# Kernel tuning notes

Measured on AMD Instinct MI355X. Metric: run time of the kernel, lower is better.

Reference implementation:

```python
import jax, jax.numpy as jnp
import numpy as np

N_NODES = 100000
N_EDGES = 3200000
DIM = 64


def setup_inputs() -> dict:
    key = jax.random.key(0)
    k1, k2, k3, k4 = jax.random.split(key, 4)
    features = jax.random.normal(k1, (N_NODES, DIM), dtype=jnp.float32)
    attn_w = jax.random.normal(k2, (2 * DIM,), dtype=jnp.float32) / np.sqrt(2 * DIM)
    src = jax.random.randint(k3, (N_EDGES,), 0, N_NODES, dtype=jnp.int32)
    dst = jax.random.randint(k4, (N_EDGES,), 0, N_NODES, dtype=jnp.int32)
    return {"features": features, "attn_w": attn_w, "src": src, "dst": dst}


def reference(features, attn_w, src, dst):
    n = features.shape[0]
    d = features.shape[1]
    a_src, a_dst = attn_w[:d], attn_w[d:]
    # Edge attention: leaky_relu(Linear(concat(h_src, h_dst))) == leaky_relu(h_src@a_src + h_dst@a_dst)
    s_src = features @ a_src  # [N]
    s_dst = features @ a_dst  # [N]
    e = jax.nn.leaky_relu(s_src[src] + s_dst[dst], negative_slope=0.01)  # [E]
    # Segment softmax over incoming edges of each destination node
    emax = jax.ops.segment_max(e, dst, num_segments=n)  # [N], -inf for isolated nodes
    ee = jnp.exp(e - emax[dst])  # [E]
    denom = jax.ops.segment_sum(ee, dst, num_segments=n)  # [N]
    alpha = ee / denom[dst]  # [E]
    # Weighted neighbor aggregation (gather src feats, scatter-add into dst)
    h = jax.ops.segment_sum(alpha[:, None] * features[src], dst, num_segments=n)  # [N, D]
    return jax.nn.elu(h)
```

## Files before the change

kernel.cpp:

```cpp
#include <hip/hip_runtime.h>
#include <math.h>

#define DIM 64
#define SCAN_BLOCK 1024
#define NB1 1024
#define TPB2 1024
#define BUCKET_BITS 7
#define BUCKET_SZ 128
#define FB_SZ 64
#define SRC_SHIFT 20
#define CAP 6144
#define CAP2 2560
#define CHUNK 12500
#define STAGE_SZ 12544
#define NSPAN 784

__device__ __forceinline__ float lrelu(float x) { return x > 0.f ? x : 0.01f * x; }
__device__ __forceinline__ float elu(float x)  { return x > 0.f ? x : expm1f(x); }

__global__ __launch_bounds__(TPB2)
void prep_scatter(const float* __restrict__ feat,
                  const float* __restrict__ attn_w,
                  float* __restrict__ s_src,
                  float* __restrict__ s_dst,
                  unsigned short* __restrict__ fbf,
                  int n_nodes,
                  const int* __restrict__ src,
                  const int* __restrict__ dst,
                  int* __restrict__ gcur,
                  int* __restrict__ bpk, int m, int nsb) {
    __shared__ int lh[NB1];
    __shared__ int bnd[NB1];
    __shared__ int cur[NB1];
    __shared__ int span_b[NSPAN];
    __shared__ int stage[STAGE_SZ];
    if (blockIdx.x < nsb) {
        int t = threadIdx.x;
        int lo = blockIdx.x * CHUNK;
        int hi = min(m, lo + CHUNK);
        int cc = hi - lo;
        int cc4 = cc >> 2;
        int nbux = (n_nodes + BUCKET_SZ - 1) >> BUCKET_BITS;
        const int4* dstv = reinterpret_cast<const int4*>(dst + lo);
        const int4* srcv = reinterpret_cast<const int4*>(src + lo);
        lh[t] = 0;
        __syncthreads();
        for (int i = t; i < cc4; i += TPB2) {
            int4 d = dstv[i];
            atomicAdd(&lh[d.x >> BUCKET_BITS], 1);
            atomicAdd(&lh[d.y >> BUCKET_BITS], 1);
            atomicAdd(&lh[d.z >> BUCKET_BITS], 1);
            atomicAdd(&lh[d.w >> BUCKET_BITS], 1);
        }
        for (int i = (cc4 << 2) + t; i < cc; i += TPB2)
            atomicAdd(&lh[dst[lo + i] >> BUCKET_BITS], 1);
        __syncthreads();
        cur[t] = lh[t];
        __syncthreads();
        for (int off = 1; off < NB1; off <<= 1) {
            int u = (t >= off) ? cur[t - off] : 0;
            __syncthreads();
            cur[t] += u;
            __syncthreads();
        }
        int excl = cur[t] - lh[t];
        bnd[t] = excl;
        int c = lh[t];
        int gb = (c > 0) ? atomicAdd(&gcur[t], c) : 0;
        lh[t]  = gb;
        cur[t] = excl;
        __syncthreads();
        if (t < nbux) {
            int s0 = (bnd[t] + 15) >> 4;
            int s1 = (bnd[t + 1] + 15) >> 4;
            for (int s = s0; s < s1; ++s) span_b[s] = t;
        }
        for (int i = t; i < cc4; i += TPB2) {
            int4 d = dstv[i];
            int4 s = srcv[i];
            int p0 = atomicAdd(&cur[d.x >> BUCKET_BITS], 1);
            stage[p0] = s.x | ((d.x & (BUCKET_SZ - 1)) << SRC_SHIFT);
            int p1 = atomicAdd(&cur[d.y >> BUCKET_BITS], 1);
            stage[p1] = s.y | ((d.y & (BUCKET_SZ - 1)) << SRC_SHIFT);
            int p2 = atomicAdd(&cur[d.z >> BUCKET_BITS], 1);
            stage[p2] = s.z | ((d.z & (BUCKET_SZ - 1)) << SRC_SHIFT);
            int p3 = atomicAdd(&cur[d.w >> BUCKET_BITS], 1);
            stage[p3] = s.w | ((d.w & (BUCKET_SZ - 1)) << SRC_SHIFT);
        }
        for (int i = (cc4 << 2) + t; i < cc; i += TPB2) {
            int d = dst[lo + i];
            int p = atomicAdd(&cur[d >> BUCKET_BITS], 1);
            stage[p] = src[lo + i] | ((d & (BUCKET_SZ - 1)) << SRC_SHIFT);
        }
        __syncthreads();
        for (int j = t; j < cc; j += TPB2) {
            int bkt = span_b[j >> 4];
            while (bnd[bkt + 1] <= j) ++bkt;
            int pos = lh[bkt] + (j - bnd[bkt]);
            if (pos < CAP)
                bpk[(size_t)bkt * CAP + pos] = stage[j];
        }
        return;
    }
    int gid  = (blockIdx.x - nsb) * blockDim.x + threadIdx.x;
    int node = gid >> 4;
    int lane = gid & 15;
    if (node >= n_nodes) return;
    const float4 f  = *reinterpret_cast<const float4*>(feat + (size_t)node * DIM + lane * 4);
    const float4 as = *reinterpret_cast<const float4*>(attn_w + lane * 4);
    const float4 ad = *reinterpret_cast<const float4*>(attn_w + DIM + lane * 4);
    float ps = f.x * as.x + f.y * as.y + f.z * as.z + f.w * as.w;
    float pd = f.x * ad.x + f.y * ad.y + f.z * ad.z + f.w * ad.w;
    uint b0 = __float_as_uint(f.x), b1 = __float_as_uint(f.y);
    uint b2 = __float_as_uint(f.z), b3 = __float_as_uint(f.w);
    ushort4 h;
    h.x = (unsigned short)((b0 + 0x7FFFu + ((b0 >> 16) & 1u)) >> 16);
    h.y = (unsigned short)((b1 + 0x7FFFu + ((b1 >> 16) & 1u)) >> 16);
    h.z = (unsigned short)((b2 + 0x7FFFu + ((b2 >> 16) & 1u)) >> 16);
    h.w = (unsigned short)((b3 + 0x7FFFu + ((b3 >> 16) & 1u)) >> 16);
    *reinterpret_cast<ushort4*>(fbf + (size_t)node * DIM + lane * 4) = h;
    for (int off = 8; off >= 1; off >>= 1) {
        ps += __shfl_xor(ps, off, 16);
        pd += __shfl_xor(pd, off, 16);
    }
    if (lane == 0) {
        s_src[node] = ps;
        s_dst[node] = pd;
    }
}

__device__ __forceinline__ void bf16x8_acc(uint4 q, float w,
                                           float& a0, float& a1, float& a2, float& a3,
                                           float& a4, float& a5, float& a6, float& a7) {
    a0 += w * __uint_as_float(q.x << 16);
    a1 += w * __uint_as_float(q.x & 0xffff0000u);
    a2 += w * __uint_as_float(q.y << 16);
    a3 += w * __uint_as_float(q.y & 0xffff0000u);
    a4 += w * __uint_as_float(q.z << 16);
    a5 += w * __uint_as_float(q.z & 0xffff0000u);
    a6 += w * __uint_as_float(q.w << 16);
    a7 += w * __uint_as_float(q.w & 0xffff0000u);
}

__global__ __launch_bounds__(256)
void sort_aggregate64(const int* __restrict__ bpk,
                      const int* __restrict__ gcur,
                      const float* __restrict__ s_src,
                      const float* __restrict__ s_dst,
                      const unsigned short* __restrict__ fbf,
                      float* __restrict__ out,
                      int n) {
    __shared__ float sdd[FB_SZ];
    __shared__ int   hist[FB_SZ];
    __shared__ int   offsl[FB_SZ];
    __shared__ int   cur[FB_SZ];
    __shared__ int   sA[FB_SZ];
    __shared__ int   sB[FB_SZ];
    __shared__ int   esrc_l[CAP2];
    __shared__ float w_l[CAP2];
    int f = blockIdx.x, t = threadIdx.x;
    int cb = f >> 1;
    int hb = (f & 1) << 6;
    int base = f * FB_SZ;
    int cnt = min(gcur[cb], CAP);
    const int*  bp  = bpk + (size_t)cb * CAP;
    const uint4* bp4 = reinterpret_cast<const uint4*>(bp);
    int cnt4 = cnt >> 2;
    if (t < FB_SZ) {
        hist[t] = 0;
        int nd = base + t;
        sdd[t] = (nd < n) ? s_dst[nd] : 0.f;
    }
    __syncthreads();
#define HPROC(pk) { int dl7_ = ((pk) >> SRC_SHIFT) & 127; \
    if ((dl7_ & 64) == hb) atomicAdd(&hist[dl7_ & 63], 1); }
    for (int e = t; e < cnt4; e += 256) {
        uint4 v = bp4[e];
        HPROC((int)v.x) HPROC((int)v.y) HPROC((int)v.z) HPROC((int)v.w)
    }
    for (int e = (cnt4 << 2) + t; e < cnt; e += 256)
        HPROC(bp[e])
    __syncthreads();
    if (t < FB_SZ) sA[t] = hist[t];
    __syncthreads();
    {
        int* pin = sA; int* pout = sB;
        for (int off = 1; off < FB_SZ; off <<= 1) {
            if (t < FB_SZ) pout[t] = (t >= off) ? pin[t] + pin[t - off] : pin[t];
            __syncthreads();
            int* tmpp = pin; pin = pout; pout = tmpp;
        }
        if (t < FB_SZ) {
            int excl = min(pin[t] - hist[t], CAP2);
            offsl[t] = excl;
            cur[t] = excl;
        }
    }
    __syncthreads();
#define SPROC(pk) { int dl7_ = ((pk) >> SRC_SHIFT) & 127; \
    if ((dl7_ & 64) == hb) { \
        int sv_ = (pk) & ((1 << SRC_SHIFT) - 1); \
        float w_ = __expf(lrelu(s_src[sv_] + sdd[dl7_ & 63])); \
        int p_ = atomicAdd(&cur[dl7_ & 63], 1); \
        if (p_ < CAP2) { esrc_l[p_] = sv_; w_l[p_] = w_; } } }
    for (int e = t; e < cnt4; e += 256) {
        uint4 v = bp4[e];
        SPROC((int)v.x) SPROC((int)v.y) SPROC((int)v.z) SPROC((int)v.w)
    }
    for (int e = (cnt4 << 2) + t; e < cnt; e += 256)
        SPROC(bp[e])
    __syncthreads();
    int l8 = t & 7, grp = t >> 3;
    const uint4* fv4 = reinterpret_cast<const uint4*>(fbf);
    for (int node = grp; node < FB_SZ; node += 32) {
        int st = offsl[node];
        int en = min(st + hist[node], CAP2);
        float a0 = 0.f, a1 = 0.f, a2 = 0.f, a3 = 0.f;
        float a4 = 0.f, a5 = 0.f, a6 = 0.f, a7 = 0.f;
        float wsum = 0.f;
        int e = st;
        for (; e + 4 <= en; e += 4) {
            int   s0 = esrc_l[e],     s1 = esrc_l[e + 1];
            int   s2 = esrc_l[e + 2], s3 = esrc_l[e + 3];
            float w0 = w_l[e],        w1 = w_l[e + 1];
            float w2 = w_l[e + 2],    w3 = w_l[e + 3];
            uint4 q0 = fv4[(size_t)s0 * 8 + l8];
            uint4 q1 = fv4[(size_t)s1 * 8 + l8];
            uint4 q2 = fv4[(size_t)s2 * 8 + l8];
            uint4 q3 = fv4[(size_t)s3 * 8 + l8];
            wsum += (w0 + w1) + (w2 + w3);
            bf16x8_acc(q0, w0, a0, a1, a2, a3, a4, a5, a6, a7);
            bf16x8_acc(q1, w1, a0, a1, a2, a3, a4, a5, a6, a7);
            bf16x8_acc(q2, w2, a0, a1, a2, a3, a4, a5, a6, a7);
            bf16x8_acc(q3, w3, a0, a1, a2, a3, a4, a5, a6, a7);
        }
        for (; e < en; e++) {
            int   s0 = esrc_l[e];
            float w0 = w_l[e];
            uint4 q0 = fv4[(size_t)s0 * 8 + l8];
            wsum += w0;
            bf16x8_acc(q0, w0, a0, a1, a2, a3, a4, a5, a6, a7);
        }
        int nd = base + node;
        if (nd < n) {
            float inv = (en > st) ? 1.f / wsum : 0.f;
            float4 o1, o2;
            o1.x = elu(a0 * inv); o1.y = elu(a1 * inv);
            o1.z = elu(a2 * inv); o1.w = elu(a3 * inv);
            o2.x = elu(a4 * inv); o2.y = elu(a5 * inv);
            o2.z = elu(a6 * inv); o2.w = elu(a7 * inv);
            float4* orow = reinterpret_cast<float4*>(out + (size_t)nd * DIM + l8 * 8);
            orow[0] = o1;
            orow[1] = o2;
        }
    }
#undef HPROC
#undef SPROC
}

__global__ void compute_scores(const float* __restrict__ feat,
                               const float* __restrict__ attn_w,
                               float* __restrict__ s_src,
                               float* __restrict__ s_dst,
                               int n_nodes) {
    int gid  = blockIdx.x * blockDim.x + threadIdx.x;
    int node = gid >> 4;
    int lane = gid & 15;
    if (node >= n_nodes) return;
    const float4 f  = *reinterpret_cast<const float4*>(feat + (size_t)node * DIM + lane * 4);
    const float4 as = *reinterpret_cast<const float4*>(attn_w + lane * 4);
    const float4 ad = *reinterpret_cast<const float4*>(attn_w + DIM + lane * 4);
    float ps = f.x * as.x + f.y * as.y + f.z * as.z + f.w * as.w;
    float pd = f.x * ad.x + f.y * ad.y + f.z * ad.z + f.w * ad.w;
    for (int off = 8; off >= 1; off >>= 1) {
        ps += __shfl_xor(ps, off, 16);
        pd += __shfl_xor(pd, off, 16);
    }
    if (lane == 0) { s_src[node] = ps; s_dst[node] = pd; }
}

__global__ void scan_level1(const int* __restrict__ in, int* __restrict__ out,
                            int* __restrict__ bsum, int n) {
    __shared__ int tmp[SCAN_BLOCK];
    int t = threadIdx.x;
    int g = blockIdx.x * SCAN_BLOCK + t;
    int v = (g < n) ? in[g] : 0;
    tmp[t] = v;
    __syncthreads();
    for (int off = 1; off < SCAN_BLOCK; off <<= 1) {
        int u = (t >= off) ? tmp[t - off] : 0;
        __syncthreads();
        tmp[t] += u;
        __syncthreads();
    }
    if (g < n) out[g] = tmp[t] - v;
    if (t == SCAN_BLOCK - 1) bsum[blockIdx.x] = tmp[t];
}

__global__ void scan_level2(int* __restrict__ bsum, int nb) {
    __shared__ int tmp[SCAN_BLOCK];
    int t = threadIdx.x;
    int v = (t < nb) ? bsum[t] : 0;
    tmp[t] = v;
    __syncthreads();
    for (int off = 1; off < SCAN_BLOCK; off <<= 1) {
        int u = (t >= off) ? tmp[t - off] : 0;
        __syncthreads();
        tmp[t] += u;
        __syncthreads();
    }
    if (t < nb) bsum[t] = tmp[t] - v;
}

__global__ void scan_level3(int* __restrict__ out, const int* __restrict__ bsum,
                            int n) {
    int g = blockIdx.x * SCAN_BLOCK + threadIdx.x;
    if (g < n) out[g] += bsum[blockIdx.x];
}

__global__ void degree_rank(const int* __restrict__ dst, int* __restrict__ deg,
                            int* __restrict__ rank, int m) {
    int i = blockIdx.x * blockDim.x + threadIdx.x;
    if (i >= m) return;
    rank[i] = atomicAdd(&deg[dst[i]], 1);
}

__global__ void scatter_src(const int* __restrict__ src, const int* __restrict__ dst,
                            const int* __restrict__ rank, const int* __restrict__ offs,
                            int* __restrict__ esrc, int m) {
    int i = blockIdx.x * blockDim.x + threadIdx.x;
    if (i >= m) return;
    esrc[offs[dst[i]] + rank[i]] = src[i];
}

__global__ void aggregate_f32(const int* __restrict__ esrc,
                              const int* __restrict__ offs,
                              const int* __restrict__ deg,
                              const float* __restrict__ s_src,
                              const float* __restrict__ s_dst,
                              const float* __restrict__ feat,
                              float* __restrict__ out, int n) {
    int gid  = blockIdx.x * blockDim.x + threadIdx.x;
    int node = gid >> 4;
    int lane = gid & 15;
    if (node >= n) return;
    int start = offs[node];
    int cnt   = deg[node];
    float sdd = s_dst[node];
    const float4* fv = reinterpret_cast<const float4*>(feat);
    float4 acc = {0.f, 0.f, 0.f, 0.f};
    float wsum = 0.f;
    for (int e = 0; e < cnt; e++) {
        int s0 = esrc[start + e];
        float w0 = __expf(lrelu(s_src[s0] + sdd));
        float4 f0 = fv[s0 * 16 + lane];
        wsum += w0;
        acc.x += w0 * f0.x; acc.y += w0 * f0.y;
        acc.z += w0 * f0.z; acc.w += w0 * f0.w;
    }
    float inv = (cnt > 0) ? 1.f / wsum : 0.f;
    float4 o;
    o.x = elu(acc.x * inv); o.y = elu(acc.y * inv);
    o.z = elu(acc.z * inv); o.w = elu(acc.w * inv);
    reinterpret_cast<float4*>(out)[node * 16 + lane] = o;
}

extern "C" void kernel_launch(void* const* d_in, const int* in_sizes, int n_in,
                              void* d_out, int out_size, void* d_ws, size_t ws_size,
                              hipStream_t stream) {
    const float* feat   = (const float*)d_in[0];
    const float* attn_w = (const float*)d_in[1];
    const int*   src    = (const int*)d_in[2];
    const int*   dst    = (const int*)d_in[3];

    const int n = in_sizes[0] / DIM;
    const int m = in_sizes[2];

    float* out = (float*)d_out;

    const int nbux = (n + BUCKET_SZ - 1) >> BUCKET_BITS;
    const int nfb  = (n + FB_SZ - 1) / FB_SZ;

    float* s_src = (float*)d_ws;
    float* s_dst = s_src + n;
    unsigned short* fbf = (unsigned short*)(s_dst + n);
    int*   gcur  = (int*)(fbf + (size_t)n * DIM);
    int*   bpk   = gcur + NB1;
    size_t need  = ((size_t)(2 + DIM / 2) * n + NB1 + (size_t)nbux * CAP)
                   * sizeof(int);

    if (ws_size >= need && nbux <= NB1) {
        hipMemsetAsync(gcur, 0, (size_t)NB1 * sizeof(int), stream);

        int nsb = (m + CHUNK - 1) / CHUNK;
        int PB  = (n * 16 + TPB2 - 1) / TPB2;
        prep_scatter<<<nsb + PB, TPB2, 0, stream>>>(
            feat, attn_w, s_src, s_dst, fbf, n, src, dst, gcur, bpk, m, nsb);

        sort_aggregate64<<<nfb, 256, 0, stream>>>(
            bpk, gcur, s_src, s_dst, fbf, out, n);
    } else {
        int* deg2  = (int*)(s_dst + n);
        int* offs2 = deg2 + n;
        int* bsum2 = offs2 + n;
        int* rank  = bsum2 + SCAN_BLOCK;
        int* esr2  = rank + m;
        int threads = n * 16;
        compute_scores<<<(threads + 255) / 256, 256, 0, stream>>>(
            feat, attn_w, s_src, s_dst, n);
        hipMemsetAsync(deg2, 0, (size_t)n * sizeof(int), stream);
        degree_rank<<<(m + 255) / 256, 256, 0, stream>>>(dst, deg2, rank, m);
        int nb2 = (n + SCAN_BLOCK - 1) / SCAN_BLOCK;
        scan_level1<<<nb2, SCAN_BLOCK, 0, stream>>>(deg2, offs2, bsum2, n);
        scan_level2<<<1, SCAN_BLOCK, 0, stream>>>(bsum2, nb2);
        scan_level3<<<nb2, SCAN_BLOCK, 0, stream>>>(offs2, bsum2, n);
        scatter_src<<<(m + 255) / 256, 256, 0, stream>>>(src, dst, rank, offs2, esr2, m);
        aggregate_f32<<<(threads + 255) / 256, 256, 0, stream>>>(
            esr2, offs2, deg2, s_src, s_dst, feat, out, n);
    }
}
```

Before: 176.5 us.

## Split fused prep kernel into edge-scatter and score kernels with smaller chunks

The combined prep_scatter kernel is split into a dedicated scatter_edges kernel and a separate prep_scores kernel launched with 256-thread blocks. The edge chunk per block is halved (CHUNK 6252), which doubles the number of scatter blocks and shrinks LDS staging so more blocks can be resident. The intent is better occupancy and load balance for the bucketing scatter. In exchange it adds a kernel launch, more global atomics on gcur, and more partial bucket segments.

```diff
diff --git a/kernel.cpp b/kernel.cpp
--- a/kernel.cpp
+++ b/kernel.cpp
@@ -4,105 +4,105 @@
 #define DIM 64
 #define SCAN_BLOCK 1024
 #define NB1 1024
-#define TPB2 1024
 #define BUCKET_BITS 7
 #define BUCKET_SZ 128
 #define FB_SZ 64
 #define SRC_SHIFT 20
 #define CAP 6144
 #define CAP2 2560
-#define CHUNK 12500
-#define STAGE_SZ 12544
-#define NSPAN 784
+#define CHUNK 6252
+#define STAGE_SZ 6272
+#define NSPAN 400
 
 __device__ __forceinline__ float lrelu(float x) { return x > 0.f ? x : 0.01f * x; }
 __device__ __forceinline__ float elu(float x)  { return x > 0.f ? x : expm1f(x); }
 
-__global__ __launch_bounds__(TPB2)
-void prep_scatter(const float* __restrict__ feat,
-                  const float* __restrict__ attn_w,
-                  float* __restrict__ s_src,
-                  float* __restrict__ s_dst,
-                  unsigned short* __restrict__ fbf,
-                  int n_nodes,
-                  const int* __restrict__ src,
-                  const int* __restrict__ dst,
-                  int* __restrict__ gcur,
-                  int* __restrict__ bpk, int m, int nsb) {
+__global__ __launch_bounds__(1024, 8)
+void scatter_edges(int n_nodes,
+                   const int* __restrict__ src,
+                   const int* __restrict__ dst,
+                   int* __restrict__ gcur,
+                   int* __restrict__ bpk, int m) {
     __shared__ int lh[NB1];
     __shared__ int bnd[NB1];
     __shared__ int cur[NB1];
     __shared__ int span_b[NSPAN];
     __shared__ int stage[STAGE_SZ];
-    if (blockIdx.x < nsb) {
-        int t = threadIdx.x;
-        int lo = blockIdx.x * CHUNK;
-        int hi = min(m, lo + CHUNK);
-        int cc = hi - lo;
-        int cc4 = cc >> 2;
-        int nbux = (n_nodes + BUCKET_SZ - 1) >> BUCKET_BITS;
-        const int4* dstv = reinterpret_cast<const int4*>(dst + lo);
-        const int4* srcv = reinterpret_cast<const int4*>(src + lo);
-        lh[t] = 0;
-        __syncthreads();
-        for (int i = t; i < cc4; i += TPB2) {
-            int4 d = dstv[i];
-            atomicAdd(&lh[d.x >> BUCKET_BITS], 1);
-            atomicAdd(&lh[d.y >> BUCKET_BITS], 1);
-            atomicAdd(&lh[d.z >> BUCKET_BITS], 1);
-            atomicAdd(&lh[d.w >> BUCKET_BITS], 1);
-        }
-        for (int i = (cc4 << 2) + t; i < cc; i += TPB2)
-            atomicAdd(&lh[dst[lo + i] >> BUCKET_BITS], 1);
-        __syncthreads();
-        cur[t] = lh[t];
-        __syncthreads();
-        for (int off = 1; off < NB1; off <<= 1) {
-            int u = (t >= off) ? cur[t - off] : 0;
-            __syncthreads();
-            cur[t] += u;
-            __syncthreads();
-        }
-        int excl = cur[t] - lh[t];
-        bnd[t] = excl;
-        int c = lh[t];
-        int gb = (c > 0) ? atomicAdd(&gcur[t], c) : 0;
-        lh[t]  = gb;
-        cur[t] = excl;
-        __syncthreads();
-        if (t < nbux) {
-            int s0 = (bnd[t] + 15) >> 4;
-            int s1 = (bnd[t + 1] + 15) >> 4;
-            for (int s = s0; s < s1; ++s) span_b[s] = t;
-        }
-        for (int i = t; i < cc4; i += TPB2) {
-            int4 d = dstv[i];
-            int4 s = srcv[i];
-            int p0 = atomicAdd(&cur[d.x >> BUCKET_BITS], 1);
-            stage[p0] = s.x | ((d.x & (BUCKET_SZ - 1)) << SRC_SHIFT);
-            int p1 = atomicAdd(&cur[d.y >> BUCKET_BITS], 1);
-            stage[p1] = s.y | ((d.y & (BUCKET_SZ - 1)) << SRC_SHIFT);
-            int p2 = atomicAdd(&cur[d.z >> BUCKET_BITS], 1);
-            stage[p2] = s.z | ((d.z & (BUCKET_SZ - 1)) << SRC_SHIFT);
-            int p3 = atomicAdd(&cur[d.w >> BUCKET_BITS], 1);
-            stage[p3] = s.w | ((d.w & (BUCKET_SZ - 1)) << SRC_SHIFT);
-        }
-        for (int i = (cc4 << 2) + t; i < cc; i += TPB2) {
-            int d = dst[lo + i];
-            int p = atomicAdd(&cur[d >> BUCKET_BITS], 1);
-            stage[p] = src[lo + i] | ((d & (BUCKET_SZ - 1)) << SRC_SHIFT);
-        }
-        __syncthreads();
-        for (int j = t; j < cc; j += TPB2) {
-            int bkt = span_b[j >> 4];
-            while (bnd[bkt + 1] <= j) ++bkt;
-            int pos = lh[bkt] + (j - bnd[bkt]);
-            if (pos < CAP)
-                bpk[(size_t)bkt * CAP + pos] = stage[j];
-        }
-        return;
-    }
-    int gid  = (blockIdx.x - nsb) * blockDim.x + threadIdx.x;
+    int t = threadIdx.x;
+    int lo = blockIdx.x * CHUNK;
+    int hi = min(m, lo + CHUNK);
+    int cc = hi - lo;
+    if (cc <= 0) return;
+    int cc4 = cc >> 2;
+    int nbux = (n_nodes + BUCKET_SZ - 1) >> BUCKET_BITS;
+    const int4* dstv = reinterpret_cast<const int4*>(dst + lo);
+    const int4* srcv = reinterpret_cast<const int4*>(src + lo);
+    lh[t] = 0;
+    __syncthreads();
+    for (int i = t; i < cc4; i += 1024) {
+        int4 d = dstv[i];
+        atomicAdd(&lh[d.x >> BUCKET_BITS], 1);
+        atomicAdd(&lh[d.y >> BUCKET_BITS], 1);
+        atomicAdd(&lh[d.z >> BUCKET_BITS], 1);
+        atomicAdd(&lh[d.w >> BUCKET_BITS], 1);
+    }
+    for (int i = (cc4 << 2) + t; i < cc; i += 1024)
+        atomicAdd(&lh[dst[lo + i] >> BUCKET_BITS], 1);
+    __syncthreads();
+    cur[t] = lh[t];
+    __syncthreads();
+    for (int off = 1; off < NB1; off <<= 1) {
+        int u = (t >= off) ? cur[t - off] : 0;
+        __syncthreads();
+        cur[t] += u;
+        __syncthreads();
+    }
+    int excl = cur[t] - lh[t];
+    bnd[t] = excl;
+    int c = lh[t];
+    int gb = (c > 0) ? atomicAdd(&gcur[t], c) : 0;
+    lh[t]  = gb;
+    cur[t] = excl;
+    __syncthreads();
+    if (t < nbux) {
+        int s0 = (bnd[t] + 15) >> 4;
+        int s1 = (bnd[t + 1] + 15) >> 4;
+        for (int s = s0; s < s1; ++s) span_b[s] = t;
+    }
+    for (int i = t; i < cc4; i += 1024) {
+        int4 d = dstv[i];
+        int4 s = srcv[i];
+        int p0 = atomicAdd(&cur[d.x >> BUCKET_BITS], 1);
+        stage[p0] = s.x | ((d.x & (BUCKET_SZ - 1)) << SRC_SHIFT);
+        int p1 = atomicAdd(&cur[d.y >> BUCKET_BITS], 1);
+        stage[p1] = s.y | ((d.y & (BUCKET_SZ - 1)) << SRC_SHIFT);
+        int p2 = atomicAdd(&cur[d.z >> BUCKET_BITS], 1);
+        stage[p2] = s.z | ((d.z & (BUCKET_SZ - 1)) << SRC_SHIFT);
+        int p3 = atomicAdd(&cur[d.w >> BUCKET_BITS], 1);
+        stage[p3] = s.w | ((d.w & (BUCKET_SZ - 1)) << SRC_SHIFT);
+    }
+    for (int i = (cc4 << 2) + t; i < cc; i += 1024) {
+        int d = dst[lo + i];
+        int p = atomicAdd(&cur[d >> BUCKET_BITS], 1);
+        stage[p] = src[lo + i] | ((d & (BUCKET_SZ - 1)) << SRC_SHIFT);
+    }
+    __syncthreads();
+    for (int j = t; j < cc; j += 1024) {
+        int bkt = span_b[j >> 4];
+        while (bnd[bkt + 1] <= j) ++bkt;
+        int pos = lh[bkt] + (j - bnd[bkt]);
+        if (pos < CAP)
+            bpk[(size_t)bkt * CAP + pos] = stage[j];
+    }
+}
+
+__global__ void prep_scores(const float* __restrict__ feat,
+                            const float* __restrict__ attn_w,
+                            float* __restrict__ s_src,
+                            float* __restrict__ s_dst,
+                            unsigned short* __restrict__ fbf,
+                            int n_nodes) {
+    int gid  = blockIdx.x * blockDim.x + threadIdx.x;
     int node = gid >> 4;
     int lane = gid & 15;
     if (node >= n_nodes) return;
@@ -393,9 +393,10 @@
         hipMemsetAsync(gcur, 0, (size_t)NB1 * sizeof(int), stream);
 
         int nsb = (m + CHUNK - 1) / CHUNK;
-        int PB  = (n * 16 + TPB2 - 1) / TPB2;
-        prep_scatter<<<nsb + PB, TPB2, 0, stream>>>(
-            feat, attn_w, s_src, s_dst, fbf, n, src, dst, gcur, bpk, m, nsb);
+        scatter_edges<<<nsb, 1024, 0, stream>>>(n, src, dst, gcur, bpk, m);
+
+        prep_scores<<<(n * 16 + 255) / 256, 256, 0, stream>>>(
+            feat, attn_w, s_src, s_dst, fbf, n);
 
         sort_aggregate64<<<nfb, 256, 0, stream>>>(
             bpk, gcur, s_src, s_dst, fbf, out, n);
```

Result: slower. 184.4 us (+4.5%).
